# Performance work log

Hardware: AMD Instinct MI355X
Metric: run time of the kernel (lower is better)

## Reference

```python
import jax, jax.numpy as jnp
import numpy as np
import math

B, S, D = 16, 1, 4096
H, KVH, HD = 32, 8, 128
MAXB, MAXS = 16, 4096
R = H // KVH  # n_rep


def _rope(t, cos, sin):
    # t: [B, S, h, HD]; cos/sin: [S, HD//2]
    tf = t.astype(jnp.float32).reshape(*t.shape[:-1], HD // 2, 2)
    a, b = tf[..., 0], tf[..., 1]
    c = cos[None, :, None, :]
    s = sin[None, :, None, :]
    out = jnp.stack([a * c - b * s, a * s + b * c], axis=-1)
    return out.reshape(t.shape).astype(t.dtype)


def setup_inputs() -> dict:
    key = jax.random.key(0)
    ks = jax.random.split(key, 9)
    scale = 1.0 / math.sqrt(D)
    ang = jax.random.uniform(ks[7], (S, HD // 2), jnp.float32) * (2.0 * np.pi)
    return {
        "x": jax.random.normal(ks[0], (B, S, D), jnp.float32),
        "start_pos": 4095,
        "freqs_cos": jnp.cos(ang),
        "freqs_sin": jnp.sin(ang),
        "cache_k": jax.random.normal(ks[1], (MAXB, MAXS, KVH, HD), jnp.float32),
        "cache_v": jax.random.normal(ks[2], (MAXB, MAXS, KVH, HD), jnp.float32),
        "wq": jax.random.normal(ks[3], (D, H * HD), jnp.float32) * scale,
        "wk": jax.random.normal(ks[4], (D, KVH * HD), jnp.float32) * scale,
        "wv": jax.random.normal(ks[5], (D, KVH * HD), jnp.float32) * scale,
        "wo": jax.random.normal(ks[6], (H * HD, D), jnp.float32) * scale,
    }


def reference(x, start_pos, freqs_cos, freqs_sin, cache_k, cache_v, wq, wk, wv, wo):
    bsz, seqlen, _ = x.shape
    xq = (x @ wq).reshape(bsz, seqlen, H, HD)
    xk = (x @ wk).reshape(bsz, seqlen, KVH, HD)
    xv = (x @ wv).reshape(bsz, seqlen, KVH, HD)
    # rotary embeddings on q and k
    xq = _rope(xq, freqs_cos, freqs_sin)
    xk = _rope(xk, freqs_cos, freqs_sin)
    # KV-cache write (start_pos is a static Python int)
    cache_k = cache_k.at[:bsz, start_pos:start_pos + seqlen].set(xk)
    cache_v = cache_v.at[:bsz, start_pos:start_pos + seqlen].set(xv)
    T = start_pos + seqlen
    keys = cache_k[:bsz, :T]    # [B, T, KVH, HD]
    values = cache_v[:bsz, :T]  # [B, T, KVH, HD]
    # GQA: group q heads as [KVH, R] instead of materializing repeated K/V
    q = xq.reshape(bsz, seqlen, KVH, R, HD)
    scores = jnp.einsum("bsgrd,btgd->bgrst", q, keys) / math.sqrt(HD)
    probs = jax.nn.softmax(scores.astype(jnp.float32), axis=-1).astype(xq.dtype)
    out = jnp.einsum("bgrst,btgd->bsgrd", probs, values)
    out = out.reshape(bsz, seqlen, H * HD)
    return out @ wo
```

## Files before the change

### kernel.cpp

```cpp
#include <hip/hip_runtime.h>
#include <hip/hip_bf16.h>
#include <math.h>

#define B 16
#define D 4096
#define H 32
#define KVH 8
#define HD 128
#define R 4
#define T 4096
#define NQKV 6144
#define NCH_A 32
#define NCH_E 32
#define CT 256
#define NCHUNK 16

#define OFF_QKV   0
#define SZ_QKV    (B*NQKV)
#define OFF_ATTN  (OFF_QKV + SZ_QKV)
#define SZ_ATTN   (B*H*HD)
#define OFF_MLO   (OFF_ATTN + SZ_ATTN)
#define SZ_MLO    (B*KVH*NCHUNK*520)
#define OFF_PART  (OFF_ATTN + SZ_ATTN)

__global__ __launch_bounds__(256) void gemv_qkv(
    const float* __restrict__ x, const float* __restrict__ wq,
    const float* __restrict__ wk, const float* __restrict__ wv,
    float* __restrict__ part) {
  int cb = blockIdx.x;
  int ch = blockIdx.y;
  int d0 = ch * 128;
  __shared__ float xT[128][20];
  for (int i = threadIdx.x; i < 128*B; i += 256) {
    int b = i >> 7;
    int d = i & 127;
    xT[d][b] = x[b*D + d0 + d];
  }
  __syncthreads();
  const float* W; int ncols, colbase, outbase;
  if (cb < 16)      { W = wq; ncols = 4096; colbase = cb*256;      outbase = colbase; }
  else if (cb < 20) { W = wk; ncols = 1024; colbase = (cb-16)*256; outbase = 4096 + colbase; }
  else              { W = wv; ncols = 1024; colbase = (cb-20)*256; outbase = 5120 + colbase; }
  int j = colbase + threadIdx.x;
  const float* wp = W + (size_t)d0*ncols + j;
  float acc[16];
  #pragma unroll
  for (int b = 0; b < 16; ++b) acc[b] = 0.f;
  for (int dd = 0; dd < 128; dd += 8) {
    float w[8];
    #pragma unroll
    for (int u = 0; u < 8; ++u) w[u] = wp[(size_t)u*ncols];
    wp += (size_t)8*ncols;
    #pragma unroll
    for (int u = 0; u < 8; ++u) {
      int d = dd + u;
      #pragma unroll
      for (int bq = 0; bq < 4; ++bq) {
        float4 xb = *(const float4*)&xT[d][bq*4];
        acc[bq*4+0] += w[u]*xb.x;
        acc[bq*4+1] += w[u]*xb.y;
        acc[bq*4+2] += w[u]*xb.z;
        acc[bq*4+3] += w[u]*xb.w;
      }
    }
  }
  int outcol = outbase + threadIdx.x;
  #pragma unroll
  for (int b = 0; b < 16; ++b) {
    part[(size_t)ch*SZ_QKV + b*NQKV + outcol] = acc[b];
  }
}

__global__ __launch_bounds__(256) void reduce_rope(
    const float* __restrict__ part, float* __restrict__ qkv,
    const float* __restrict__ fc, const float* __restrict__ fs) {
  int i = blockIdx.x*256 + threadIdx.x;
  int flat = i*2;
  float2 s = make_float2(0.f, 0.f);
  for (int c = 0; c < NCH_A; ++c) {
    float2 v = *(const float2*)&part[(size_t)c*SZ_QKV + flat];
    s.x += v.x; s.y += v.y;
  }
  int col = flat % NQKV;
  if (col < 5120) {
    int jj = (col & 127) >> 1;
    float c = fc[jj], sn = fs[jj];
    float ox = s.x*c - s.y*sn;
    float oy = s.x*sn + s.y*c;
    if (col < 4096) { ox *= 0.08838834764831845f; oy *= 0.08838834764831845f; }
    s.x = ox; s.y = oy;
  }
  *(float2*)&qkv[flat] = s;
}

__global__ __launch_bounds__(256) void attn_kernel(
    const float* __restrict__ qkv, const float* __restrict__ cache_k,
    const float* __restrict__ cache_v, float* __restrict__ mlo) {
  int chunk = blockIdx.x, g = blockIdx.y, b = blockIdx.z;
  int tid = threadIdx.x, wave = tid >> 6, lane = tid & 63;
  __shared__ float4 s_lds4[CT];
  __shared__ float o_lds[4][4][HD];

  {
    int sub = lane & 7;
    int rloc = lane >> 3;
    float4 qreg[4][4];
    const float* qp = qkv + b*NQKV + g*R*HD;
    #pragma unroll
    for (int h = 0; h < 4; ++h)
      #pragma unroll
      for (int i = 0; i < 4; ++i)
        qreg[h][i] = *(const float4*)(qp + h*HD + (i*8 + sub)*4);

    #pragma unroll 2
    for (int p = 0; p < 8; ++p) {
      int row = wave*64 + p*8 + rloc;
      int tA = chunk*CT + row;
      const float* kp = (tA == T-1) ? &qkv[b*NQKV + 4096 + g*HD]
                        : &cache_k[(((size_t)b*T + tA)*KVH + g)*HD];
      float4 kreg[4];
      #pragma unroll
      for (int i = 0; i < 4; ++i) kreg[i] = ((const float4*)kp)[i*8 + sub];
      float sA[4] = {0.f,0.f,0.f,0.f};
      #pragma unroll
      for (int i = 0; i < 4; ++i) {
        #pragma unroll
        for (int h = 0; h < 4; ++h) {
          sA[h] += kreg[i].x*qreg[h][i].x + kreg[i].y*qreg[h][i].y
                 + kreg[i].z*qreg[h][i].z + kreg[i].w*qreg[h][i].w;
        }
      }
      #pragma unroll
      for (int h = 0; h < 4; ++h) {
        sA[h] += __shfl_xor(sA[h], 1);
        sA[h] += __shfl_xor(sA[h], 2);
        sA[h] += __shfl_xor(sA[h], 4);
      }
      if (sub == 0) s_lds4[row] = make_float4(sA[0], sA[1], sA[2], sA[3]);
    }
  }
  __syncthreads();

  {
    int h = wave;
    float v[4]; float m = -1e30f;
    #pragma unroll
    for (int i = 0; i < 4; ++i) {
      v[i] = ((const float*)&s_lds4[lane + i*64])[h];
      m = fmaxf(m, v[i]);
    }
    for (int off = 32; off > 0; off >>= 1) m = fmaxf(m, __shfl_xor(m, off));
    float l = 0.f;
    #pragma unroll
    for (int i = 0; i < 4; ++i) {
      float p = __expf(v[i] - m);
      ((float*)&s_lds4[lane + i*64])[h] = p;
      l += p;
    }
    for (int off = 32; off > 0; off >>= 1) l += __shfl_xor(l, off);
    if (lane == 0) {
      size_t base = ((size_t)(b*KVH + g)*NCHUNK + chunk)*520;
      mlo[base + h] = m;
      mlo[base + 4 + h] = l;
    }
  }
  __syncthreads();

  {
    int sub = lane & 31;
    int rhalf = lane >> 5;
    float4 acc4[4];
    #pragma unroll
    for (int h = 0; h < 4; ++h) acc4[h] = make_float4(0.f,0.f,0.f,0.f);
    int rbase = wave*64;
    #pragma unroll 2
    for (int bt = 0; bt < 8; ++bt) {
      float4 vreg[4];
      #pragma unroll
      for (int i = 0; i < 4; ++i) {
        int tl = rbase + bt*8 + i*2 + rhalf;
        int t = chunk*CT + tl;
        const float* vrow = (t == T-1) ? &qkv[b*NQKV + 5120 + g*HD]
                           : &cache_v[(((size_t)b*T + t)*KVH + g)*HD];
        vreg[i] = *(const float4*)&vrow[sub*4];
      }
      #pragma unroll
      for (int i = 0; i < 4; ++i) {
        int tl = rbase + bt*8 + i*2 + rhalf;
        float4 p = s_lds4[tl];
        acc4[0].x += p.x*vreg[i].x; acc4[0].y += p.x*vreg[i].y;
        acc4[0].z += p.x*vreg[i].z; acc4[0].w += p.x*vreg[i].w;
        acc4[1].x += p.y*vreg[i].x; acc4[1].y += p.y*vreg[i].y;
        acc4[1].z += p.y*vreg[i].z; acc4[1].w += p.y*vreg[i].w;
        acc4[2].x += p.z*vreg[i].x; acc4[2].y += p.z*vreg[i].y;
        acc4[2].z += p.z*vreg[i].z; acc4[2].w += p.z*vreg[i].w;
        acc4[3].x += p.w*vreg[i].x; acc4[3].y += p.w*vreg[i].y;
        acc4[3].z += p.w*vreg[i].z; acc4[3].w += p.w*vreg[i].w;
      }
    }
    #pragma unroll
    for (int h = 0; h < 4; ++h) {
      acc4[h].x += __shfl_xor(acc4[h].x, 32);
      acc4[h].y += __shfl_xor(acc4[h].y, 32);
      acc4[h].z += __shfl_xor(acc4[h].z, 32);
      acc4[h].w += __shfl_xor(acc4[h].w, 32);
    }
    if (rhalf == 0) {
      #pragma unroll
      for (int h = 0; h < 4; ++h)
        *(float4*)&o_lds[wave][h][sub*4] = acc4[h];
    }
  }
  __syncthreads();
  size_t base = ((size_t)(b*KVH + g)*NCHUNK + chunk)*520;
  for (int oi = tid; oi < 512; oi += 256) {
    int h = oi >> 7, d = oi & 127;
    float s = 0.f;
    #pragma unroll
    for (int w = 0; w < 4; ++w) s += o_lds[w][h][d];
    mlo[base + 8 + oi] = s;
  }
}

__global__ __launch_bounds__(128) void combine_kernel(
    const float* __restrict__ mlo, float* __restrict__ attn) {
  int g = blockIdx.x, b = blockIdx.y;
  int d = threadIdx.x;
  #pragma unroll
  for (int h = 0; h < 4; ++h) {
    float mc[NCHUNK], lc[NCHUNK];
    float mg = -1e30f;
    #pragma unroll
    for (int c = 0; c < NCHUNK; ++c) {
      size_t base = ((size_t)(b*KVH + g)*NCHUNK + c)*520;
      mc[c] = mlo[base + h];
      lc[c] = mlo[base + 4 + h];
      mg = fmaxf(mg, mc[c]);
    }
    float lg = 0.f, o = 0.f;
    #pragma unroll
    for (int c = 0; c < NCHUNK; ++c) {
      size_t base = ((size_t)(b*KVH + g)*NCHUNK + c)*520;
      float f = __expf(mc[c] - mg);
      lg += f*lc[c];
      o  += f*mlo[base + 8 + h*HD + d];
    }
    attn[b*D + (g*R + h)*HD + d] = o / lg;
  }
}

__global__ __launch_bounds__(256) void gemv_out(
    const float* __restrict__ attn, const float* __restrict__ wo,
    float* __restrict__ part) {
  int cb = blockIdx.x;
  int ch = blockIdx.y;
  int d0 = ch * 128;
  __shared__ float xT[128][20];
  for (int i = threadIdx.x; i < 128*B; i += 256) {
    int b = i >> 7;
    int d = i & 127;
    xT[d][b] = attn[b*D + d0 + d];
  }
  __syncthreads();
  int j = cb*256 + threadIdx.x;
  const float* wp = wo + (size_t)d0*D + j;
  float acc[16];
  #pragma unroll
  for (int b = 0; b < 16; ++b) acc[b] = 0.f;
  for (int dd = 0; dd < 128; dd += 8) {
    float w[8];
    #pragma unroll
    for (int u = 0; u < 8; ++u) w[u] = wp[(size_t)u*D];
    wp += (size_t)8*D;
    #pragma unroll
    for (int u = 0; u < 8; ++u) {
      int d = dd + u;
      #pragma unroll
      for (int bq = 0; bq < 4; ++bq) {
        float4 xb = *(const float4*)&xT[d][bq*4];
        acc[bq*4+0] += w[u]*xb.x;
        acc[bq*4+1] += w[u]*xb.y;
        acc[bq*4+2] += w[u]*xb.z;
        acc[bq*4+3] += w[u]*xb.w;
      }
    }
  }
  #pragma unroll
  for (int b = 0; b < 16; ++b) {
    part[(size_t)ch*SZ_ATTN + b*D + j] = acc[b];
  }
}

__global__ __launch_bounds__(256) void reduce_part(
    const float* __restrict__ part, float* __restrict__ out, int n, int nch) {
  int i = (blockIdx.x*256 + threadIdx.x)*4;
  if (i >= n) return;
  float4 s = make_float4(0.f,0.f,0.f,0.f);
  for (int c = 0; c < nch; ++c) {
    float4 v = *(const float4*)&part[(size_t)c*n + i];
    s.x += v.x; s.y += v.y; s.z += v.z; s.w += v.w;
  }
  *(float4*)&out[i] = s;
}

extern "C" void kernel_launch(void* const* d_in, const int* in_sizes, int n_in,
                              void* d_out, int out_size, void* d_ws, size_t ws_size,
                              hipStream_t stream) {
  const float* x  = (const float*)d_in[0];
  const float* fc = (const float*)d_in[2];
  const float* fs = (const float*)d_in[3];
  const float* ck = (const float*)d_in[4];
  const float* cv = (const float*)d_in[5];
  const float* wq = (const float*)d_in[6];
  const float* wk = (const float*)d_in[7];
  const float* wv = (const float*)d_in[8];
  const float* wo = (const float*)d_in[9];
  float* out  = (float*)d_out;
  float* ws   = (float*)d_ws;
  float* qkv  = ws + OFF_QKV;
  float* attn = ws + OFF_ATTN;
  float* mlo  = ws + OFF_MLO;
  float* part = ws + OFF_PART;

  gemv_qkv<<<dim3(24, NCH_A), 256, 0, stream>>>(x, wq, wk, wv, part);
  reduce_rope<<<dim3(SZ_QKV/512), 256, 0, stream>>>(part, qkv, fc, fs);
  attn_kernel<<<dim3(NCHUNK, KVH, B), 256, 0, stream>>>(qkv, ck, cv, mlo);
  combine_kernel<<<dim3(KVH, B), 128, 0, stream>>>(mlo, attn);
  gemv_out<<<dim3(16, NCH_E), 256, 0, stream>>>(attn, wo, part);
  reduce_part<<<dim3(SZ_ATTN/1024), 256, 0, stream>>>(part, out, SZ_ATTN, NCH_E);
}
```

Measured before the change: 179.1 us.

## Stage K loads through padded LDS with register double-buffering in attention score loop

```diff
diff --git a/kernel.cpp b/kernel.cpp
--- a/kernel.cpp
+++ b/kernel.cpp
@@ -100,10 +100,12 @@
   int tid = threadIdx.x, wave = tid >> 6, lane = tid & 63;
   __shared__ float4 s_lds4[CT];
   __shared__ float o_lds[4][4][HD];
+  __shared__ float4 ktile[4*8*35];
+#define KT(w,r,s) ktile[((w)*8+(r))*35+(s)]
 
   {
-    int sub = lane & 7;
-    int rloc = lane >> 3;
+    int sub = lane & 7, rloc = lane >> 3;
+    int pos = lane & 31, rhalf = lane >> 5;
     float4 qreg[4][4];
     const float* qp = qkv + b*NQKV + g*R*HD;
     #pragma unroll
@@ -112,22 +114,38 @@
       for (int i = 0; i < 4; ++i)
         qreg[h][i] = *(const float4*)(qp + h*HD + (i*8 + sub)*4);
 
-    #pragma unroll 2
-    for (int p = 0; p < 8; ++p) {
-      int row = wave*64 + p*8 + rloc;
-      int tA = chunk*CT + row;
-      const float* kp = (tA == T-1) ? &qkv[b*NQKV + 4096 + g*HD]
-                        : &cache_k[(((size_t)b*T + tA)*KVH + g)*HD];
-      float4 kreg[4];
-      #pragma unroll
-      for (int i = 0; i < 4; ++i) kreg[i] = ((const float4*)kp)[i*8 + sub];
+    const float* knew = qkv + b*NQKV + 4096 + g*HD;
+    int tbase = chunk*CT + wave*64;
+    float4 cur[4];
+    #pragma unroll
+    for (int ii = 0; ii < 4; ++ii) {
+      int t = tbase + ii*2 + rhalf;
+      const float* kp = (t == T-1) ? knew
+                        : &cache_k[(((size_t)b*T + t)*KVH + g)*HD];
+      cur[ii] = *(const float4*)&kp[pos*4];
+    }
+    for (int bt = 0; bt < 8; ++bt) {
+      float4 nxt[4];
+      if (bt < 7) {
+        #pragma unroll
+        for (int ii = 0; ii < 4; ++ii) {
+          int t = tbase + (bt+1)*8 + ii*2 + rhalf;
+          const float* kp = (t == T-1) ? knew
+                            : &cache_k[(((size_t)b*T + t)*KVH + g)*HD];
+          nxt[ii] = *(const float4*)&kp[pos*4];
+        }
+      }
+      #pragma unroll
+      for (int ii = 0; ii < 4; ++ii)
+        KT(wave, ii*2 + rhalf, pos) = cur[ii];
       float sA[4] = {0.f,0.f,0.f,0.f};
       #pragma unroll
       for (int i = 0; i < 4; ++i) {
+        float4 kf = KT(wave, rloc, i*8 + sub);
         #pragma unroll
         for (int h = 0; h < 4; ++h) {
-          sA[h] += kreg[i].x*qreg[h][i].x + kreg[i].y*qreg[h][i].y
-                 + kreg[i].z*qreg[h][i].z + kreg[i].w*qreg[h][i].w;
+          sA[h] += kf.x*qreg[h][i].x + kf.y*qreg[h][i].y
+                 + kf.z*qreg[h][i].z + kf.w*qreg[h][i].w;
         }
       }
       #pragma unroll
@@ -136,7 +154,9 @@
         sA[h] += __shfl_xor(sA[h], 2);
         sA[h] += __shfl_xor(sA[h], 4);
       }
-      if (sub == 0) s_lds4[row] = make_float4(sA[0], sA[1], sA[2], sA[3]);
+      if (sub == 0) s_lds4[wave*64 + bt*8 + rloc] = make_float4(sA[0], sA[1], sA[2], sA[3]);
+      #pragma unroll
+      for (int ii = 0; ii < 4; ++ii) cur[ii] = nxt[ii];
     }
   }
   __syncthreads();
```

After: 180.3 us. No clear change (+0.6%).
